# Kernel optimization log

Measured on AMD Instinct MI355X. Metric: run time of the kernel, lower is better.

Reference implementation:

```python
import jax, jax.numpy as jnp
import numpy as np
import math

B, T, C = 2, 2048, 2048
NH, L = 16, 128  # n_head, LCompression


def setup_inputs() -> dict:
    key = jax.random.key(0)
    ks = jax.random.split(key, 7)
    s = 0.02
    return {
        "x": jax.random.normal(ks[0], (B, T, C), dtype=jnp.float32),
        # latent: Linear(n_embd -> LComp), stored as [in, out]
        "W_lat": jax.random.normal(ks[1], (C, L), dtype=jnp.float32) * s,
        "b_lat": jnp.zeros((L,), dtype=jnp.float32),
        # Wd: Linear(n_embd -> n_head*LComp)
        "W_d": jax.random.normal(ks[2], (C, NH * L), dtype=jnp.float32) * s,
        "b_d": jnp.zeros((NH * L,), dtype=jnp.float32),
        # c_proj: Linear(n_head*LComp -> n_embd)
        "W_proj": jax.random.normal(ks[3], (NH * L, C), dtype=jnp.float32) * s,
        "b_proj": jnp.zeros((C,), dtype=jnp.float32),
    }


def reference(x, W_lat, b_lat, W_d, b_d, W_proj, b_proj):
    Bx, Tx, Cx = x.shape
    # shared low-rank latent, used as both K and V (identical across heads)
    k = x @ W_lat + b_lat                                   # [B,T,L]
    q = (x @ W_d + b_d).reshape(Bx, Tx, NH, L)              # [B,T,H,L]
    q = jnp.transpose(q, (0, 2, 1, 3))                      # [B,H,T,L]
    scale = 1.0 / math.sqrt(L)
    # scores against the head-shared latent (no per-head K expansion)
    att = jnp.einsum("bhtl,bsl->bhts", q, k) * scale        # [B,H,T,T]
    causal = jnp.tril(jnp.ones((Tx, Tx), dtype=bool))
    att = jnp.where(causal[None, None], att, -jnp.inf)
    att = jax.nn.softmax(att, axis=-1)
    y = jnp.einsum("bhts,bsl->bhtl", att, k)                # [B,H,T,L]
    y = jnp.transpose(y, (0, 2, 1, 3)).reshape(Bx, Tx, NH * L)
    return y @ W_proj + b_proj                              # [B,T,C]
```

## Files before the change

### kernel.cpp

```cpp
#include <hip/hip_runtime.h>
#include <hip/hip_bf16.h>

#define B_   2
#define T_   2048
#define C_   2048
#define NH_  16
#define L_   128
#define NKQ  2176
#define MTOK 4096
#define SCALE2_ 0.12753785792696073f

typedef short short8 __attribute__((ext_vector_type(8)));
typedef float f32x4  __attribute__((ext_vector_type(4)));
typedef float f32x16 __attribute__((ext_vector_type(16)));

#define GLD16(gp, lp) __builtin_amdgcn_global_load_lds(                      \
    (const __attribute__((address_space(1))) void*)(gp),                     \
    (__attribute__((address_space(3))) void*)(lp), 16, 0, 0)

__device__ __forceinline__ unsigned short f2bf(float f) {
  union { float f; unsigned u; } x; x.f = f;
  unsigned r = x.u + 0x7fffu + ((x.u >> 16) & 1u);
  return (unsigned short)(r >> 16);
}

__global__ __launch_bounds__(256) void prep_all(
    const float* __restrict__ x, const float* __restrict__ W_lat,
    const float* __restrict__ W_d, const float* __restrict__ W_proj,
    const float* __restrict__ b_lat, const float* __restrict__ b_d,
    unsigned short* __restrict__ x_bf, unsigned short* __restrict__ BtCat,
    unsigned short* __restrict__ WprojT, float* __restrict__ biascat) {
  __shared__ float tile[32][33];
  int bid = blockIdx.x;
  const int tid = threadIdx.x;

  if (bid < 8192) {
    int i = bid * 1024 + tid * 4;
    float4 v = *(const float4*)(x + i);
    ushort4 o;
    o.x = f2bf(v.x); o.y = f2bf(v.y); o.z = f2bf(v.z); o.w = f2bf(v.w);
    *(ushort4*)(x_bf + i) = o;
    return;
  }
  bid -= 8192;

  const float* W; unsigned short* Wt; int K, N; float mul; int nbx;
  if (bid < 256) {
    W = W_lat; Wt = BtCat; K = C_; N = L_; mul = 1.f; nbx = 4;
  } else if (bid < 256 + 4096) {
    bid -= 256;
    W = W_d; Wt = BtCat + (size_t)L_ * C_; K = C_; N = NH_ * L_; mul = SCALE2_; nbx = 64;
  } else if (bid < 256 + 8192) {
    bid -= 256 + 4096;
    W = W_proj; Wt = WprojT; K = NH_ * L_; N = C_; mul = 1.f; nbx = 64;
  } else {
    int i = (bid - (256 + 8192)) * 256 + tid;
    if (i < L_) biascat[i] = b_lat[i];
    else if (i < NKQ) biascat[i] = b_d[i - L_] * SCALE2_;
    return;
  }

  const int bx = (bid % nbx) * 32, by = (bid / nbx) * 32;
  const int tx = tid & 31, ty = tid >> 5;
  #pragma unroll
  for (int i2 = 0; i2 < 4; i2++)
    tile[ty + i2 * 8][tx] = W[(size_t)(by + ty + i2 * 8) * N + bx + tx];
  __syncthreads();
  #pragma unroll
  for (int i2 = 0; i2 < 4; i2++)
    Wt[(size_t)(bx + ty + i2 * 8) * K + by + tx] = f2bf(tile[tx][ty + i2 * 8] * mul);
}

__global__ __launch_bounds__(256) void gemm_bt_bias(
    const unsigned short* __restrict__ A,
    const unsigned short* __restrict__ Bt,
    const float* __restrict__ bias,
    unsigned short* __restrict__ Cb,
    float* __restrict__ Cf,
    unsigned short* __restrict__ KlTout,
    int M, int N, int K) {
  __shared__ __align__(16) unsigned short As[2][128 * 32];
  __shared__ __align__(16) unsigned short Bs[2][128 * 32];
  const int tid  = threadIdx.x;
  const int wave = tid >> 6, lane = tid & 63;
  const int lcol = lane & 15, quad = lane >> 4;
  const int lin = blockIdx.y * gridDim.x + blockIdx.x;
  const int xcd = lin & 7, idx = lin >> 3;
  const int mpx = gridDim.x >> 3;
  const int m0 = (xcd * mpx + idx % mpx) * 128;
  const int n0 = (idx / mpx) * 128;
  const int wm = (wave >> 1) * 64, wn = (wave & 1) * 64;
  const int lrow = lane >> 2, lchunk = (lane & 3) * 8;
  const int rb = wave * 32;

  f32x4 acc[4][4];
  #pragma unroll
  for (int i = 0; i < 4; i++)
    #pragma unroll
    for (int j = 0; j < 4; j++) acc[i][j] = (f32x4){0.f, 0.f, 0.f, 0.f};

  const int nk = K >> 5;
  GLD16(&A [(size_t)(m0 + rb      + lrow) * K + lchunk], &As[0][ rb       * 32]);
  GLD16(&A [(size_t)(m0 + rb + 16 + lrow) * K + lchunk], &As[0][(rb + 16) * 32]);
  GLD16(&Bt[(size_t)(n0 + rb      + lrow) * K + lchunk], &Bs[0][ rb       * 32]);
  GLD16(&Bt[(size_t)(n0 + rb + 16 + lrow) * K + lchunk], &Bs[0][(rb + 16) * 32]);

  for (int kt = 0; kt < nk; ++kt) {
    const int cur = kt & 1;
    __syncthreads();

    if (kt + 1 < nk) {
      const int kc = (kt + 1) << 5;
      GLD16(&A [(size_t)(m0 + rb      + lrow) * K + kc + lchunk], &As[cur ^ 1][ rb       * 32]);
      GLD16(&A [(size_t)(m0 + rb + 16 + lrow) * K + kc + lchunk], &As[cur ^ 1][(rb + 16) * 32]);
      GLD16(&Bt[(size_t)(n0 + rb      + lrow) * K + kc + lchunk], &Bs[cur ^ 1][ rb       * 32]);
      GLD16(&Bt[(size_t)(n0 + rb + 16 + lrow) * K + kc + lchunk], &Bs[cur ^ 1][(rb + 16) * 32]);
    }

    short8 af[4], bfr[4];
    #pragma unroll
    for (int i = 0; i < 4; i++)
      af[i] = *(const short8*)&As[cur][(wm + i * 16 + lcol) * 32 + quad * 8];
    #pragma unroll
    for (int j = 0; j < 4; j++)
      bfr[j] = *(const short8*)&Bs[cur][(wn + j * 16 + lcol) * 32 + quad * 8];
    #pragma unroll
    for (int i = 0; i < 4; i++)
      #pragma unroll
      for (int j = 0; j < 4; j++)
        acc[i][j] = __builtin_amdgcn_mfma_f32_16x16x32_bf16(af[i], bfr[j], acc[i][j], 0, 0, 0);
  }

  #pragma unroll
  for (int i = 0; i < 4; i++) {
    #pragma unroll
    for (int j = 0; j < 4; j++) {
      int col = n0 + wn + j * 16 + lcol;
      float bv = bias[col];
      #pragma unroll
      for (int r = 0; r < 4; r++) {
        int row = m0 + wm + i * 16 + quad * 4 + r;
        float v = acc[i][j][r] + bv;
        if (Cf) Cf[(size_t)row * N + col] = v;
        else {
          unsigned short hv = f2bf(v);
          Cb[(size_t)row * N + col] = hv;
          if (KlTout && n0 == 0)
            KlTout[((size_t)(row >> 11) * L_ + col) * T_ + (row & 2047)] = hv;
        }
      }
    }
  }
}

__global__ __launch_bounds__(256, 2) void attn_mla(
    const unsigned short* __restrict__ kq,
    const unsigned short* __restrict__ KlT,
    unsigned short* __restrict__ y) {
  __shared__ __align__(16) unsigned short Kr[2][64 * 128];
  __shared__ __align__(16) unsigned short Kt[2][128 * 64];
  __shared__ __align__(16) float ls[4][32];

  const int tid  = threadIdx.x;
  const int wave = tid >> 6, lane = tid & 63;
  const int l31 = lane & 31, hf = lane >> 5;
  const int n    = blockIdx.x;
  const int slot = n >> 8, c = n & 255;
  const int hg   = c >> 5, qi = c & 31;
  const int b    = hg >> 2;
  const int h    = (hg & 3) * 4 + wave;
  const int qt32 = slot ? qi : (63 - qi);
  const size_t rowbase = (size_t)b * T_;
  const int q0 = qt32 * 32;

  short8 qf[8];
  {
    const unsigned short* qp =
        kq + (rowbase + q0 + l31) * NKQ + L_ + h * L_ + hf * 8;
    #pragma unroll
    for (int kc = 0; kc < 8; kc++)
      qf[kc] = *(const short8*)(qp + kc * 16);
  }

  f32x16 acco[4];
  #pragma unroll
  for (int nb = 0; nb < 4; nb++)
    #pragma unroll
    for (int r = 0; r < 16; r++) acco[nb][r] = 0.f;
  float lsum = 0.f;

  const int nt = (qt32 >> 1) + 1;

  #pragma unroll
  for (int kk = 0; kk < 4; kk++) {
    int r0 = wave * 16 + kk * 4;
    int rg = r0 + (lane >> 4);
    int cl = ((lane & 15) ^ (rg & 15)) * 8;
    GLD16(kq + (rowbase + rg) * NKQ + cl, &Kr[0][r0 * 128]);
  }
  #pragma unroll
  for (int kk = 0; kk < 4; kk++) {
    int r0 = wave * 32 + kk * 8;
    int rg = r0 + (lane >> 3);
    int cl = ((lane & 7) ^ (rg & 7) ^ (((rg >> 3) & 1) << 2)) * 8;
    GLD16(KlT + ((size_t)b * L_ + rg) * T_ + cl, &Kt[0][r0 * 64]);
  }

  for (int ts = 0; ts < nt; ts++) {
    const int cur = ts & 1;
    __syncthreads();

    if (ts + 1 < nt) {
      const int s1 = (ts + 1) * 64;
      #pragma unroll
      for (int kk = 0; kk < 4; kk++) {
        int r0 = wave * 16 + kk * 4;
        int rg = r0 + (lane >> 4);
        int cl = ((lane & 15) ^ (rg & 15)) * 8;
        GLD16(kq + (rowbase + s1 + rg) * NKQ + cl, &Kr[cur ^ 1][r0 * 128]);
      }
      #pragma unroll
      for (int kk = 0; kk < 4; kk++) {
        int r0 = wave * 32 + kk * 8;
        int rg = r0 + (lane >> 3);
        int cl = ((lane & 7) ^ (rg & 7) ^ (((rg >> 3) & 1) << 2)) * 8;
        GLD16(KlT + ((size_t)b * L_ + rg) * T_ + s1 + cl, &Kt[cur ^ 1][r0 * 64]);
      }
    }

    const unsigned short* Krc = &Kr[cur][0];
    const unsigned short* Ktc = &Kt[cur][0];

    f32x16 accs[2];
    #pragma unroll
    for (int sb = 0; sb < 2; sb++)
      #pragma unroll
      for (int r = 0; r < 16; r++) accs[sb][r] = 0.f;
    __builtin_amdgcn_s_setprio(1);
    #pragma unroll
    for (int kc = 0; kc < 8; kc++)
      #pragma unroll
      for (int sb = 0; sb < 2; sb++) {
        short8 kf = *(const short8*)&Krc[(sb * 32 + l31) * 128 +
                                          (((2 * kc + hf) ^ (l31 & 15)) * 8)];
        accs[sb] = __builtin_amdgcn_mfma_f32_32x32x16_bf16(kf, qf[kc], accs[sb], 0, 0, 0);
      }
    __builtin_amdgcn_s_setprio(0);

    const bool diag = (ts == nt - 1);
    const int qg = (qt32 & 1) * 32 + l31;
    #pragma unroll
    for (int sb = 0; sb < 2; sb++)
      #pragma unroll
      for (int r = 0; r < 16; r++) {
        float v = accs[sb][r];
        int s64 = sb * 32 + (r & 3) + 8 * (r >> 2) + 4 * hf;
        if (diag && s64 > qg) v = -1e30f;
        accs[sb][r] = __builtin_amdgcn_exp2f(v);
      }

    #pragma unroll
    for (int kc = 0; kc < 4; kc++) {
      const int sb = kc >> 1;
      const int t0 = (kc & 1) * 2;
      unsigned w00, w01, w10, w11;
      asm("v_cvt_pk_bf16_f32 %0, %1, %2" : "=v"(w00)
          : "v"(accs[sb][4 * t0 + 0]), "v"(accs[sb][4 * t0 + 1]));
      asm("v_cvt_pk_bf16_f32 %0, %1, %2" : "=v"(w01)
          : "v"(accs[sb][4 * t0 + 2]), "v"(accs[sb][4 * t0 + 3]));
      asm("v_cvt_pk_bf16_f32 %0, %1, %2" : "=v"(w10)
          : "v"(accs[sb][4 * t0 + 4]), "v"(accs[sb][4 * t0 + 5]));
      asm("v_cvt_pk_bf16_f32 %0, %1, %2" : "=v"(w11)
          : "v"(accs[sb][4 * t0 + 6]), "v"(accs[sb][4 * t0 + 7]));
      asm volatile("v_permlane32_swap_b32 %0, %1" : "+v"(w00), "+v"(w10));
      asm volatile("v_permlane32_swap_b32 %0, %1" : "+v"(w01), "+v"(w11));
      union { short8 s; unsigned u[4]; } F;
      F.u[0] = w00; F.u[1] = w01; F.u[2] = w10; F.u[3] = w11;
      #pragma unroll
      for (int w = 0; w < 4; w++) {
        lsum += __uint_as_float(F.u[w] << 16);
        lsum += __uint_as_float(F.u[w] & 0xffff0000u);
      }
      __builtin_amdgcn_s_setprio(1);
      #pragma unroll
      for (int nb = 0; nb < 4; nb++) {
        int rowv = nb * 32 + l31;
        short8 vf = *(const short8*)&Ktc[rowv * 64 +
            (((2 * kc + hf) ^ (rowv & 7) ^ (((rowv >> 3) & 1) << 2)) * 8)];
        acco[nb] = __builtin_amdgcn_mfma_f32_32x32x16_bf16(F.s, vf, acco[nb], 0, 0, 0);
      }
      __builtin_amdgcn_s_setprio(0);
    }
  }

  lsum += __shfl_xor(lsum, 32, 64);
  if (lane < 32) ls[wave][l31] = 1.f / lsum;
  __syncthreads();
  f32x4 rv[4];
  #pragma unroll
  for (int t = 0; t < 4; t++)
    rv[t] = *(const f32x4*)&ls[wave][8 * t + 4 * hf];

  #pragma unroll
  for (int nb = 0; nb < 4; nb++)
    #pragma unroll
    for (int r = 0; r < 16; r++) {
      int q = q0 + (r & 3) + 8 * (r >> 2) + 4 * hf;
      int l = nb * 32 + l31;
      y[(rowbase + q) * (NH_ * L_) + h * L_ + l] =
          f2bf(acco[nb][r] * rv[r >> 2][r & 3]);
    }
}

extern "C" void kernel_launch(void* const* d_in, const int* in_sizes, int n_in,
                              void* d_out, int out_size, void* d_ws, size_t ws_size,
                              hipStream_t stream) {
  const float* x      = (const float*)d_in[0];
  const float* W_lat  = (const float*)d_in[1];
  const float* b_lat  = (const float*)d_in[2];
  const float* W_d    = (const float*)d_in[3];
  const float* b_d    = (const float*)d_in[4];
  const float* W_proj = (const float*)d_in[5];
  const float* b_proj = (const float*)d_in[6];
  float* out = (float*)d_out;

  unsigned short* x_bf   = (unsigned short*)d_ws;
  unsigned short* BtCat  = x_bf   + (size_t)MTOK * C_;
  unsigned short* WprojT = BtCat  + (size_t)NKQ * C_;
  unsigned short* kqbuf  = WprojT + (size_t)C_ * (NH_ * L_);
  unsigned short* ybuf   = kqbuf  + (size_t)MTOK * NKQ;
  unsigned short* KlT    = ybuf   + (size_t)MTOK * (NH_ * L_);
  float*          biascat = (float*)(KlT + (size_t)B_ * L_ * T_);

  prep_all<<<16649, 256, 0, stream>>>(x, W_lat, W_d, W_proj, b_lat, b_d,
                                      x_bf, BtCat, WprojT, biascat);
  gemm_bt_bias<<<dim3(MTOK / 128, NKQ / 128), 256, 0, stream>>>(
      x_bf, BtCat, biascat, kqbuf, nullptr, KlT, MTOK, NKQ, C_);
  attn_mla<<<512, 256, 0, stream>>>(kqbuf, KlT, ybuf);
  gemm_bt_bias<<<dim3(MTOK / 128, C_ / 128), 256, 0, stream>>>(
      ybuf, WprojT, b_proj, nullptr, out, nullptr, MTOK, C_, C_);
}
```

Baseline: 280.8 us.

## Add 8-wave ping-pong output-projection GEMM and coarsen x conversion blocks

Replaces the output projection GEMM with a new 512-thread kernel using 256x128 tiles. It double-buffers LDS loads via global_load_lds and splits each k-step into four barrier-separated phases that interleave next-tile loads with MFMA work at raised priority. Separately, the x-to-bf16 conversion now handles four float4 chunks per thread, so fewer blocks are launched. The aim is better overlap of memory and matrix work in the final GEMM, at the cost of hand-tuned vmcnt waits that must match the load ordering.

```diff
diff --git a/kernel.cpp b/kernel.cpp
--- a/kernel.cpp
+++ b/kernel.cpp
@@ -17,6 +17,8 @@
 #define GLD16(gp, lp) __builtin_amdgcn_global_load_lds(                      \
     (const __attribute__((address_space(1))) void*)(gp),                     \
     (__attribute__((address_space(3))) void*)(lp), 16, 0, 0)
+
+#define VMW(n) asm volatile("s_waitcnt vmcnt(" #n ")" ::: "memory")
 
 __device__ __forceinline__ unsigned short f2bf(float f) {
   union { float f; unsigned u; } x; x.f = f;
@@ -34,15 +36,19 @@
   int bid = blockIdx.x;
   const int tid = threadIdx.x;
 
-  if (bid < 8192) {
-    int i = bid * 1024 + tid * 4;
-    float4 v = *(const float4*)(x + i);
-    ushort4 o;
-    o.x = f2bf(v.x); o.y = f2bf(v.y); o.z = f2bf(v.z); o.w = f2bf(v.w);
-    *(ushort4*)(x_bf + i) = o;
+  if (bid < 2048) {
+    int base = bid * 4096 + tid * 4;
+    #pragma unroll
+    for (int it = 0; it < 4; it++) {
+      int i = base + it * 1024;
+      float4 v = *(const float4*)(x + i);
+      ushort4 o;
+      o.x = f2bf(v.x); o.y = f2bf(v.y); o.z = f2bf(v.z); o.w = f2bf(v.w);
+      *(ushort4*)(x_bf + i) = o;
+    }
     return;
   }
-  bid -= 8192;
+  bid -= 2048;
 
   const float* W; unsigned short* Wt; int K, N; float mul; int nbx;
   if (bid < 256) {
@@ -153,6 +159,122 @@
   }
 }
 
+__global__ __launch_bounds__(512, 2) void gemm2_8p(
+    const unsigned short* __restrict__ A,
+    const unsigned short* __restrict__ Bt,
+    const float* __restrict__ bias,
+    float* __restrict__ Cf,
+    int M, int N, int K) {
+  __shared__ __align__(16) unsigned short As[2][256 * 64];
+  __shared__ __align__(16) unsigned short Bs[2][128 * 64];
+  const int tid  = threadIdx.x;
+  const int wave = tid >> 6, lane = tid & 63;
+  const int lcol = lane & 15, quad = lane >> 4;
+  const int m0 = blockIdx.x * 256, n0 = blockIdx.y * 128;
+  const int wr = (wave >> 1) * 32, wc = (wave & 1) * 32;
+  const int srow = lane >> 3, schunk = lane & 7;
+  const int scl = (schunk ^ srow) * 8;
+
+  f32x4 acc[2][2][2][2];
+  #pragma unroll
+  for (int a = 0; a < 2; a++)
+    #pragma unroll
+    for (int b = 0; b < 2; b++)
+      #pragma unroll
+      for (int c = 0; c < 2; c++)
+        #pragma unroll
+        for (int d = 0; d < 2; d++) acc[a][b][c][d] = (f32x4){0.f, 0.f, 0.f, 0.f};
+
+  const int nk = K >> 6;
+
+  auto stA = [&](int kt, int buf, int u) {
+    int rg = u * 64 + wave * 8 + srow;
+    GLD16(&A[(size_t)(m0 + rg) * K + (kt << 6) + scl], &As[buf][(u * 64 + wave * 8) * 64]);
+  };
+  auto stB = [&](int kt, int buf, int u) {
+    int rg = u * 64 + wave * 8 + srow;
+    GLD16(&Bt[(size_t)(n0 + rg) * K + (kt << 6) + scl], &Bs[buf][(u * 64 + wave * 8) * 64]);
+  };
+
+#define READS8(MH, NH)                                                        \
+  short8 af[2][2], bfr[2][2];                                                 \
+  _Pragma("unroll") for (int mf = 0; mf < 2; mf++)                            \
+    _Pragma("unroll") for (int kk = 0; kk < 2; kk++) {                        \
+      int ra = (MH) * 128 + wr + mf * 16 + lcol;                              \
+      af[mf][kk] = *(const short8*)&As[cur][ra * 64 +                         \
+                     (((kk * 4 + quad) ^ (lcol & 7)) * 8)];                   \
+    }                                                                         \
+  _Pragma("unroll") for (int nf = 0; nf < 2; nf++)                            \
+    _Pragma("unroll") for (int kk = 0; kk < 2; kk++) {                        \
+      int rb2 = (NH) * 64 + wc + nf * 16 + lcol;                              \
+      bfr[nf][kk] = *(const short8*)&Bs[cur][rb2 * 64 +                       \
+                      (((kk * 4 + quad) ^ (lcol & 7)) * 8)];                  \
+    }
+
+#define MFMAS8(MH, NH)                                                        \
+  __builtin_amdgcn_s_setprio(1);                                              \
+  _Pragma("unroll") for (int kk = 0; kk < 2; kk++)                            \
+    _Pragma("unroll") for (int mf = 0; mf < 2; mf++)                          \
+      _Pragma("unroll") for (int nf = 0; nf < 2; nf++)                        \
+        acc[MH][NH][mf][nf] = __builtin_amdgcn_mfma_f32_16x16x32_bf16(        \
+            af[mf][kk], bfr[nf][kk], acc[MH][NH][mf][nf], 0, 0, 0);           \
+  __builtin_amdgcn_s_setprio(0);
+
+  stA(0, 0, 0); stA(0, 0, 1); stB(0, 0, 0); stB(0, 0, 1); stA(0, 0, 2); stA(0, 0, 3);
+
+  for (int kt = 0; kt < nk; ++kt) {
+    const int cur = kt & 1, nxt = cur ^ 1;
+    const bool last = (kt == nk - 1);
+    const int kn = kt + 1;
+
+    VMW(3);
+    __builtin_amdgcn_s_barrier(); __builtin_amdgcn_sched_barrier(0);
+    {
+      READS8(0, 0);
+      if (!last) { stA(kn, nxt, 0); stA(kn, nxt, 1); }
+      MFMAS8(0, 0);
+    }
+    if (last) { VMW(2); } else { VMW(4); }
+    __builtin_amdgcn_s_barrier(); __builtin_amdgcn_sched_barrier(0);
+    {
+      READS8(0, 1);
+      if (!last) stB(kn, nxt, 0);
+      MFMAS8(0, 1);
+    }
+    if (last) { VMW(0); } else { VMW(3); }
+    __builtin_amdgcn_s_barrier(); __builtin_amdgcn_sched_barrier(0);
+    {
+      READS8(1, 0);
+      if (!last) stB(kn, nxt, 1);
+      MFMAS8(1, 0);
+    }
+    if (!last) { VMW(4); }
+    __builtin_amdgcn_s_barrier(); __builtin_amdgcn_sched_barrier(0);
+    {
+      READS8(1, 1);
+      if (!last) { stA(kn, nxt, 2); stA(kn, nxt, 3); }
+      MFMAS8(1, 1);
+    }
+  }
+
+  #pragma unroll
+  for (int mh = 0; mh < 2; mh++)
+    #pragma unroll
+    for (int nh = 0; nh < 2; nh++)
+      #pragma unroll
+      for (int nf = 0; nf < 2; nf++) {
+        int col = n0 + nh * 64 + wc + nf * 16 + lcol;
+        float bv = bias[col];
+        #pragma unroll
+        for (int mf = 0; mf < 2; mf++)
+          #pragma unroll
+          for (int r = 0; r < 4; r++) {
+            int row = m0 + mh * 128 + wr + mf * 16 + quad * 4 + r;
+            Cf[(size_t)row * N + col] = acc[mh][nh][mf][nf][r] + bv;
+          }
+      }
+}
+
 __global__ __launch_bounds__(256, 2) void attn_mla(
     const unsigned short* __restrict__ kq,
     const unsigned short* __restrict__ KlT,
@@ -332,11 +454,11 @@
   unsigned short* KlT    = ybuf   + (size_t)MTOK * (NH_ * L_);
   float*          biascat = (float*)(KlT + (size_t)B_ * L_ * T_);
 
-  prep_all<<<16649, 256, 0, stream>>>(x, W_lat, W_d, W_proj, b_lat, b_d,
+  prep_all<<<10505, 256, 0, stream>>>(x, W_lat, W_d, W_proj, b_lat, b_d,
                                       x_bf, BtCat, WprojT, biascat);
   gemm_bt_bias<<<dim3(MTOK / 128, NKQ / 128), 256, 0, stream>>>(
       x_bf, BtCat, biascat, kqbuf, nullptr, KlT, MTOK, NKQ, C_);
   attn_mla<<<512, 256, 0, stream>>>(kqbuf, KlT, ybuf);
-  gemm_bt_bias<<<dim3(MTOK / 128, C_ / 128), 256, 0, stream>>>(
-      ybuf, WprojT, b_proj, nullptr, out, nullptr, MTOK, C_, C_);
-}
+  gemm2_8p<<<dim3(MTOK / 256, C_ / 128), 512, 0, stream>>>(
+      ybuf, WprojT, b_proj, out, MTOK, C_, C_);
+}
```

Result: slower. 290.8 us (+3.6%).
